# Performance work log

Hardware: AMD Instinct MI355X
Metric: run time of the kernel (lower is better)

The kernel has to match this reference:

```python
import jax, jax.numpy as jnp
import numpy as np
from jax import lax

B, S, D, T = 128, 512, 512, 64
OUT = 3


def setup_inputs() -> dict:
    key = jax.random.key(0)
    ks = jax.random.split(key, 16)
    sd = 0.05
    return {
        "e_all": jax.random.normal(ks[0], (B, S, D), jnp.float32),
        "e_last": jax.random.normal(ks[1], (1, B, D), jnp.float32),
        "target": jax.random.normal(ks[2], (B, T, OUT), jnp.float32),
        # attention params
        "Wa": jax.random.normal(ks[3], (D, D), jnp.float32) * sd,
        "ba": jnp.zeros((D,), jnp.float32),
        "Ua": jax.random.normal(ks[4], (D, D), jnp.float32) * sd,
        "bu": jnp.zeros((D,), jnp.float32),
        "Va_w": jax.random.normal(ks[5], (1, D), jnp.float32) * sd,
        "Va_b": jnp.zeros((1,), jnp.float32),
        # GRU params (PyTorch layout: [3D, in], gates order r,z,n)
        "W_ih": jax.random.normal(ks[6], (3 * D, D + OUT), jnp.float32) * sd,
        "b_ih": jnp.zeros((3 * D,), jnp.float32),
        "W_hh": jax.random.normal(ks[7], (3 * D, D), jnp.float32) * sd,
        "b_hh": jnp.zeros((3 * D,), jnp.float32),
        # output projection
        "W_out": jax.random.normal(ks[8], (OUT, D), jnp.float32) * sd,
        "b_out": jnp.zeros((OUT,), jnp.float32),
    }


def reference(e_all, e_last, target, Wa, ba, Ua, bu, Va_w, Va_b,
              W_ih, b_ih, W_hh, b_hh, W_out, b_out):
    # Precompute Ua(keys): keys are fixed across timesteps (same math as per-step).
    Uk = jnp.einsum('bsd,ed->bse', e_all, Ua) + bu        # [B,S,D]
    va = Va_w[0]                                          # [D]

    def step(h, x):
        # h: [B,D] decoder hidden; x: [B,3] decoder input (dropout is eval/identity)
        q = h @ Wa.T + ba                                  # [B,D]
        scores = jnp.einsum('bsd,d->bs', jnp.tanh(q[:, None, :] + Uk), va) + Va_b[0]
        w = jax.nn.softmax(scores, axis=-1)                # [B,S]
        ctx = jnp.einsum('bs,bsd->bd', w, e_all)           # [B,D]
        gin = jnp.concatenate([ctx, x], axis=-1)           # [B,D+3]  (attn first)
        gi = gin @ W_ih.T + b_ih                           # [B,3D]
        gh = h @ W_hh.T + b_hh                             # [B,3D]
        i_r, i_z, i_n = jnp.split(gi, 3, axis=-1)
        h_r, h_z, h_n = jnp.split(gh, 3, axis=-1)
        r = jax.nn.sigmoid(i_r + h_r)
        z = jax.nn.sigmoid(i_z + h_z)
        n = jnp.tanh(i_n + r * h_n)
        h_new = (1.0 - z) * n + z * h                      # [B,D]
        out = h_new @ W_out.T + b_out                      # [B,3]
        return h_new, (out, w)

    # teacher forcing: step 0 sees zeros, step i sees target[:, i-1]
    xs = jnp.concatenate([jnp.zeros((1, B, OUT), e_all.dtype),
                          jnp.swapaxes(target[:, :T - 1, :], 0, 1)], axis=0)  # [T,B,3]
    hT, (outs, attns) = lax.scan(step, e_last[0], xs)
    d_outputs = jnp.swapaxes(outs, 0, 1)     # [B,T,3]
    cross_attn = jnp.swapaxes(attns, 0, 1)   # [B,T,S]
    return d_outputs, hT[None], cross_attn
```

## Files before the change

kernel.cpp:

```cpp
#include <hip/hip_runtime.h>
#include <cstdint>

constexpr int BB = 128;
constexpr int SS = 512;
constexpr int DD = 512;
constexpr int TT = 64;
constexpr int OO = 3;

typedef __attribute__((ext_vector_type(8))) short bf16x8;
typedef __attribute__((ext_vector_type(4))) float f32x4;

__device__ __forceinline__ float tanh_fast(float x) {
  float e = __expf(2.0f * x);
  return 1.0f - 2.0f / (e + 1.0f);
}
__device__ __forceinline__ float sigmoid_fast(float x) {
  return 1.0f / (1.0f + __expf(-x));
}
__device__ __forceinline__ unsigned short f2bf(float f) {
  uint32_t u = __float_as_uint(f);
  uint32_t r = (u + 0x7FFFu + ((u >> 16) & 1u)) >> 16;
  return (unsigned short)r;
}
__device__ __forceinline__ float2 bfx2(uint32_t u) {
  float2 r;
  r.x = __uint_as_float(u << 16);
  r.y = __uint_as_float(u & 0xFFFF0000u);
  return r;
}

template<int BM, int BN, int BK, int TM, int TN>
__device__ __forceinline__ void gemm_body(
    const float* __restrict__ A, int lda,
    const float* __restrict__ Bw, int ldb,
    const float* __restrict__ bias,
    float* __restrict__ C, int ldc, int K) {
  constexpr int TX = BN / TN, TY = BM / TM;
  static_assert(TX * TY == 256, "tile/thread mismatch");
  __shared__ float As[BK][BM + 4];
  __shared__ float Bs[BK][BN + 4];
  const int tid = threadIdx.x;
  const int bm = blockIdx.y * BM, bn = blockIdx.x * BN;
  const int tx = tid % TX, ty = tid / TX;
  float acc[TM][TN];
#pragma unroll
  for (int i = 0; i < TM; ++i)
#pragma unroll
    for (int j = 0; j < TN; ++j) acc[i][j] = 0.f;

  for (int k0 = 0; k0 < K; k0 += BK) {
#pragma unroll
    for (int i = 0; i < BM * BK / 256; ++i) {
      int idx = tid + i * 256;
      int m = idx / BK, k = idx % BK;
      As[k][m] = A[(size_t)(bm + m) * lda + k0 + k];
    }
#pragma unroll
    for (int i = 0; i < BN * BK / 256; ++i) {
      int idx = tid + i * 256;
      int n = idx / BK, k = idx % BK;
      Bs[k][n] = Bw[(size_t)(bn + n) * ldb + k0 + k];
    }
    __syncthreads();
#pragma unroll
    for (int k = 0; k < BK; ++k) {
      float ra[TM], rb[TN];
#pragma unroll
      for (int i = 0; i < TM; ++i) ra[i] = As[k][ty * TM + i];
#pragma unroll
      for (int j = 0; j < TN; ++j) rb[j] = Bs[k][tx * TN + j];
#pragma unroll
      for (int i = 0; i < TM; ++i)
#pragma unroll
        for (int j = 0; j < TN; ++j) acc[i][j] += ra[i] * rb[j];
    }
    __syncthreads();
  }
#pragma unroll
  for (int i = 0; i < TM; ++i) {
    int m = bm + ty * TM + i;
#pragma unroll
    for (int j = 0; j < TN; ++j) {
      int n = bn + tx * TN + j;
      C[(size_t)m * ldc + n] = acc[i][j] + bias[n];
    }
  }
}

__global__ __launch_bounds__(256) void gemm_uk_mfma(
    const unsigned short* __restrict__ A, const unsigned short* __restrict__ Bw,
    const float* __restrict__ bias, unsigned short* __restrict__ Uk) {
  __shared__ unsigned short Asb[128 * 40];
  __shared__ unsigned short Bsb[128 * 40];
  const int tid = threadIdx.x;
  const int m0 = blockIdx.y * 128, n0 = blockIdx.x * 128;
  const int w = tid >> 6, l = tid & 63;
  const int wr = w >> 1, wc = w & 1;
  const int lm = l & 15, kg = l >> 4;

  f32x4 acc[4][4] = {};

  for (int kc = 0; kc < 512; kc += 32) {
    uint4 av[2], bv[2];
#pragma unroll
    for (int p = 0; p < 2; ++p) {
      int u = tid + p * 256;
      int r = u >> 2, ko = (u & 3) * 8;
      av[p] = *(const uint4*)(A + (size_t)(m0 + r) * 512 + kc + ko);
      bv[p] = *(const uint4*)(Bw + (size_t)(n0 + r) * 512 + kc + ko);
    }
    __syncthreads();
#pragma unroll
    for (int p = 0; p < 2; ++p) {
      int u = tid + p * 256;
      int r = u >> 2, ko = (u & 3) * 8;
      *(uint4*)&Asb[r * 40 + ko] = av[p];
      *(uint4*)&Bsb[r * 40 + ko] = bv[p];
    }
    __syncthreads();
    bf16x8 af[4], bfr[4];
#pragma unroll
    for (int i = 0; i < 4; ++i) {
      af[i]  = *(const bf16x8*)&Asb[(wr * 64 + i * 16 + lm) * 40 + kg * 8];
      bfr[i] = *(const bf16x8*)&Bsb[(wc * 64 + i * 16 + lm) * 40 + kg * 8];
    }
#pragma unroll
    for (int i = 0; i < 4; ++i)
#pragma unroll
      for (int j = 0; j < 4; ++j)
        acc[i][j] = __builtin_amdgcn_mfma_f32_16x16x32_bf16(af[i], bfr[j],
                                                            acc[i][j], 0, 0, 0);
  }

  const int row_base = m0 + wr * 64;
  const int col_base = n0 + wc * 64;
#pragma unroll
  for (int j = 0; j < 4; ++j) {
    const int col = col_base + j * 16 + lm;
    const float bu = bias[col];
#pragma unroll
    for (int i = 0; i < 4; ++i) {
      const int r0 = row_base + i * 16 + kg * 4;
#pragma unroll
      for (int rr = 0; rr < 4; ++rr)
        Uk[(size_t)(r0 + rr) * 512 + col] = f2bf(acc[i][j][rr] + bu);
    }
  }
}

__global__ __launch_bounds__(256) void conv_bf(const float* __restrict__ in,
                                               unsigned short* __restrict__ outp) {
  size_t idx = ((size_t)blockIdx.x * 256 + threadIdx.x) * 8;
  const float4* p = (const float4*)(in + idx);
  float4 a = p[0], b = p[1];
  uint4 r;
  r.x = f2bf(a.x) | ((uint32_t)f2bf(a.y) << 16);
  r.y = f2bf(a.z) | ((uint32_t)f2bf(a.w) << 16);
  r.z = f2bf(b.x) | ((uint32_t)f2bf(b.y) << 16);
  r.w = f2bf(b.z) | ((uint32_t)f2bf(b.w) << 16);
  *(uint4*)(outp + idx) = r;
}

__global__ void prep_wcat(const float* __restrict__ Wa,
                          const float* __restrict__ Whh,
                          uint32_t* __restrict__ Wcat) {
  int idx = blockIdx.x * 256 + threadIdx.x;
  int k = idx >> 10, j2 = idx & 1023;
  int j0 = 2 * j2;
  float v0 = (j0 < DD) ? Wa[(size_t)j0 * DD + k] : Whh[(size_t)(j0 - DD) * DD + k];
  float v1 = (j0 + 1 < DD) ? Wa[(size_t)(j0 + 1) * DD + k]
                           : Whh[(size_t)(j0 + 1 - DD) * DD + k];
  Wcat[idx] = (uint32_t)f2bf(v0) | ((uint32_t)f2bf(v1) << 16);
}

__global__ void prep_bcat(const float* __restrict__ ba,
                          const float* __restrict__ bhh,
                          float* __restrict__ bcat) {
  int j = blockIdx.x * 256 + threadIdx.x;
  bcat[j] = (j < DD) ? ba[j] : bhh[j - DD];
}

__device__ __forceinline__ void qgh_gemm(
    const float* __restrict__ hn_sh, const uint32_t* __restrict__ Wcat,
    const float* __restrict__ bcat, float* __restrict__ q,
    float* __restrict__ gh, int b, int tid) {
  float2 acc = {0.f, 0.f};
#pragma unroll 8
  for (int k = 0; k < DD; ++k) {
    float2 wv = bfx2(Wcat[(size_t)k * 1024 + tid]);
    float hv = hn_sh[k];
    acc.x += hv * wv.x;
    acc.y += hv * wv.y;
  }
  const int j0 = 2 * tid;
  acc.x += bcat[j0];
  acc.y += bcat[j0 + 1];
  if (j0 < DD) {
    q[(size_t)b * DD + j0] = acc.x;
    q[(size_t)b * DD + j0 + 1] = acc.y;
  } else {
    gh[(size_t)b * 3 * DD + j0 - DD] = acc.x;
    gh[(size_t)b * 3 * DD + j0 + 1 - DD] = acc.y;
  }
}

__global__ __launch_bounds__(1024) void qgh_init(
    const float* __restrict__ e_last, const uint32_t* __restrict__ Wcat,
    const float* __restrict__ bcat, float* __restrict__ h,
    float* __restrict__ q, float* __restrict__ gh) {
  const int b = blockIdx.x, tid = threadIdx.x;
  __shared__ float hn[DD];
  if (tid < DD) {
    float v = e_last[(size_t)b * DD + tid];
    hn[tid] = v;
    h[(size_t)b * DD + tid] = v;
  }
  __syncthreads();
  qgh_gemm(hn, Wcat, bcat, q, gh, b, tid);
}

__global__ __launch_bounds__(256) void attn_scores(
    const unsigned short* __restrict__ Uk_bf, const float* __restrict__ q,
    const float* __restrict__ va, const float* __restrict__ vb_p,
    float* __restrict__ scores) {
  const int b = blockIdx.y;
  const int s0 = blockIdx.x * 64;
  __shared__ float4 shq[DD / 4];
  __shared__ float4 shva[DD / 4];
  const int tid = threadIdx.x;
  if (tid < DD / 4) {
    shq[tid] = ((const float4*)(q + (size_t)b * DD))[tid];
    shva[tid] = ((const float4*)va)[tid];
  }
  __syncthreads();
  const float vb = vb_p[0];
  const int g = tid >> 4, l = tid & 15;
#pragma unroll
  for (int i = 0; i < 4; ++i) {
    const int s = s0 + 16 * i + g;
    const uint4* row = (const uint4*)(Uk_bf + ((size_t)b * SS + s) * DD);
    float acc = 0.f;
#pragma unroll
    for (int jj = 0; jj < 4; ++jj) {
      const int slot = l + 16 * jj;
      uint4 u = row[slot];
      float4 q0 = shq[slot * 2], q1 = shq[slot * 2 + 1];
      float4 v0 = shva[slot * 2], v1 = shva[slot * 2 + 1];
      float2 e0 = bfx2(u.x), e1 = bfx2(u.y), e2 = bfx2(u.z), e3 = bfx2(u.w);
      acc += v0.x * tanh_fast(q0.x + e0.x);
      acc += v0.y * tanh_fast(q0.y + e0.y);
      acc += v0.z * tanh_fast(q0.z + e1.x);
      acc += v0.w * tanh_fast(q0.w + e1.y);
      acc += v1.x * tanh_fast(q1.x + e2.x);
      acc += v1.y * tanh_fast(q1.y + e2.y);
      acc += v1.z * tanh_fast(q1.z + e3.x);
      acc += v1.w * tanh_fast(q1.w + e3.y);
    }
#pragma unroll
    for (int off = 8; off; off >>= 1) acc += __shfl_down(acc, off, 16);
    if (l == 0) scores[(size_t)b * SS + s] = acc + vb;
  }
}

__global__ __launch_bounds__(256) void attn_ctx(
    const unsigned short* __restrict__ e_bf, const float* __restrict__ scores,
    float* __restrict__ ctx, float* __restrict__ attn_out, int t) {
  const int b = blockIdx.y, dc = blockIdx.x;
  __shared__ float w[SS];
  __shared__ float red[8];
  __shared__ float part[16][132];
  const int tid = threadIdx.x;

  float v0 = scores[(size_t)b * SS + tid];
  float v1 = scores[(size_t)b * SS + 256 + tid];
  float m = fmaxf(v0, v1);
#pragma unroll
  for (int off = 32; off; off >>= 1) m = fmaxf(m, __shfl_xor(m, off));
  if ((tid & 63) == 0) red[tid >> 6] = m;
  __syncthreads();
  m = fmaxf(fmaxf(red[0], red[1]), fmaxf(red[2], red[3]));
  float e0 = __expf(v0 - m), e1 = __expf(v1 - m);
  float ss = e0 + e1;
#pragma unroll
  for (int off = 32; off; off >>= 1) ss += __shfl_xor(ss, off);
  __syncthreads();
  if ((tid & 63) == 0) red[tid >> 6] = ss;
  __syncthreads();
  const float inv = 1.f / (red[0] + red[1] + red[2] + red[3]);
  float w0 = e0 * inv, w1 = e1 * inv;
  w[tid] = w0;
  w[tid + 256] = w1;
  if (dc == 0) {
    float* ao = attn_out + ((size_t)b * TT + t) * SS;
    ao[tid] = w0;
    ao[tid + 256] = w1;
  }
  __syncthreads();

  {
    const int sl = tid & 15, sg = tid >> 4;
    const unsigned short* eb = e_bf + (size_t)b * SS * DD + dc * 128 + sl * 8;
    float a0 = 0.f, a1 = 0.f, a2 = 0.f, a3 = 0.f;
    float a4 = 0.f, a5 = 0.f, a6 = 0.f, a7 = 0.f;
    for (int s = sg * 32; s < sg * 32 + 32; ++s) {
      uint4 u = *(const uint4*)(eb + (size_t)s * DD);
      float ws = w[s];
      float2 p0 = bfx2(u.x), p1 = bfx2(u.y), p2 = bfx2(u.z), p3 = bfx2(u.w);
      a0 += ws * p0.x; a1 += ws * p0.y;
      a2 += ws * p1.x; a3 += ws * p1.y;
      a4 += ws * p2.x; a5 += ws * p2.y;
      a6 += ws * p3.x; a7 += ws * p3.y;
    }
    float* pr = &part[sg][sl * 8];
    pr[0] = a0; pr[1] = a1; pr[2] = a2; pr[3] = a3;
    pr[4] = a4; pr[5] = a5; pr[6] = a6; pr[7] = a7;
  }
  __syncthreads();
  if (tid < 128) {
    const int sl = tid >> 3, c = tid & 7;
    float r = 0.f;
#pragma unroll
    for (int sg = 0; sg < 16; ++sg) r += part[sg][sl * 8 + c];
    ctx[(size_t)b * DD + dc * 128 + sl * 8 + c] = r;
  }
}

__global__ __launch_bounds__(256) void gi_gemm(
    const float* __restrict__ ctx, const float* __restrict__ W_ih,
    const float* __restrict__ bih, float* __restrict__ gi) {
  gemm_body<16, 64, 32, 1, 4>(ctx, DD, W_ih, DD + OO, bih, gi, 3 * DD, DD);
}

__global__ __launch_bounds__(1024) void update_fused(
    const float* __restrict__ gi, float* __restrict__ gh,
    float* __restrict__ h,
    const float* __restrict__ W_ih, const float* __restrict__ target,
    const float* __restrict__ W_out, const float* __restrict__ b_out,
    const uint32_t* __restrict__ Wcat, const float* __restrict__ bcat,
    float* __restrict__ q,
    float* __restrict__ out_d, float* __restrict__ out_hT, int t) {
  const int b = blockIdx.x, tid = threadIdx.x;
  __shared__ float hn[DD];
  const int wid = tid >> 6, lane = tid & 63;

  if (tid < DD) {
    const int d = tid;
    float x0 = 0.f, x1 = 0.f, x2 = 0.f;
    if (t > 0) {
      const float* xp = target + ((size_t)b * TT + (t - 1)) * OO;
      x0 = xp[0]; x1 = xp[1]; x2 = xp[2];
    }
    const float* gib = gi + (size_t)b * 3 * DD;
    const float* ghb = gh + (size_t)b * 3 * DD;
    const float* w0 = W_ih + (size_t)d * (DD + OO) + DD;
    const float* w1 = W_ih + (size_t)(DD + d) * (DD + OO) + DD;
    const float* w2 = W_ih + (size_t)(2 * DD + d) * (DD + OO) + DD;
    float ir  = gib[d]          + x0 * w0[0] + x1 * w0[1] + x2 * w0[2];
    float iz  = gib[DD + d]     + x0 * w1[0] + x1 * w1[1] + x2 * w1[2];
    float in_ = gib[2 * DD + d] + x0 * w2[0] + x1 * w2[1] + x2 * w2[2];
    float r = sigmoid_fast(ir + ghb[d]);
    float z = sigmoid_fast(iz + ghb[DD + d]);
    float n = tanh_fast(in_ + r * ghb[2 * DD + d]);
    float hp = h[(size_t)b * DD + d];
    float hnew = (1.f - z) * n + z * hp;
    h[(size_t)b * DD + d] = hnew;
    hn[d] = hnew;
    if (t == TT - 1) out_hT[(size_t)b * DD + d] = hnew;
  }
  __syncthreads();

  if (wid < OO) {
    const float* wrow = W_out + (size_t)wid * DD;
    float acc = 0.f;
    for (int i = lane; i < DD; i += 64) acc += hn[i] * wrow[i];
#pragma unroll
    for (int off = 32; off; off >>= 1) acc += __shfl_xor(acc, off);
    if (lane == 0) out_d[((size_t)b * TT + t) * OO + wid] = acc + b_out[wid];
  }

  qgh_gemm(hn, Wcat, bcat, q, gh, b, tid);
}

extern "C" void kernel_launch(void* const* d_in, const int* in_sizes, int n_in,
                              void* d_out, int out_size, void* d_ws, size_t ws_size,
                              hipStream_t stream) {
  const float* e_all  = (const float*)d_in[0];
  const float* e_last = (const float*)d_in[1];
  const float* target = (const float*)d_in[2];
  const float* Wa     = (const float*)d_in[3];
  const float* ba     = (const float*)d_in[4];
  const float* Ua     = (const float*)d_in[5];
  const float* bu     = (const float*)d_in[6];
  const float* Va_w   = (const float*)d_in[7];
  const float* Va_b   = (const float*)d_in[8];
  const float* W_ih   = (const float*)d_in[9];
  const float* b_ih   = (const float*)d_in[10];
  const float* W_hh   = (const float*)d_in[11];
  const float* b_hh   = (const float*)d_in[12];
  const float* W_out  = (const float*)d_in[13];
  const float* b_out  = (const float*)d_in[14];

  float* out      = (float*)d_out;
  float* out_d    = out;
  float* out_hT   = out + (size_t)BB * TT * OO;
  float* out_attn = out_hT + (size_t)BB * DD;

  char* wsB = (char*)d_ws;
  unsigned short* Uk_bf = (unsigned short*)wsB;
  unsigned short* e_bf  = (unsigned short*)(wsB + (size_t)BB * SS * DD * 2);
  uint32_t* Wcat = (uint32_t*)(wsB + (size_t)BB * SS * DD * 4);
  unsigned short* Ua_bf = (unsigned short*)(wsB + (size_t)BB * SS * DD * 4 +
                                            (size_t)DD * 2048 * 2);
  float* fws = (float*)((char*)Ua_bf + (size_t)DD * DD * 2);
  float* bcat   = fws;
  float* scores = bcat + 2048;
  float* q    = scores + (size_t)BB * SS;
  float* h    = q + (size_t)BB * DD;
  float* ctx  = h + (size_t)BB * DD;
  float* gi   = ctx + (size_t)BB * DD;
  float* gh   = gi + (size_t)BB * 3 * DD;

  prep_wcat<<<(DD * 1024) / 256, 256, 0, stream>>>(Wa, W_hh, Wcat);
  prep_bcat<<<2048 / 256, 256, 0, stream>>>(ba, b_hh, bcat);
  conv_bf<<<(BB * SS * DD) / (8 * 256), 256, 0, stream>>>(e_all, e_bf);
  conv_bf<<<(DD * DD) / (8 * 256), 256, 0, stream>>>(Ua, Ua_bf);
  gemm_uk_mfma<<<dim3(DD / 128, (BB * SS) / 128), 256, 0, stream>>>(
      e_bf, Ua_bf, bu, Uk_bf);
  qgh_init<<<BB, 1024, 0, stream>>>(e_last, Wcat, bcat, h, q, gh);

  for (int t = 0; t < TT; ++t) {
    attn_scores<<<dim3(SS / 64, BB), 256, 0, stream>>>(Uk_bf, q, Va_w, Va_b,
                                                       scores);
    attn_ctx<<<dim3(4, BB), 256, 0, stream>>>(e_bf, scores, ctx, out_attn, t);
    gi_gemm<<<dim3(3 * DD / 64, BB / 16), 256, 0, stream>>>(ctx, W_ih, b_ih, gi);
    update_fused<<<BB, 1024, 0, stream>>>(gi, gh, h, W_ih, target, W_out, b_out,
                                          Wcat, bcat, q, out_d, out_hT, t);
  }
}
```

Before: 5.621 ms.

## Fuse per-step attention, q/gh projection and GRU into two kernels per timestep

Restructures the per-timestep pipeline from four launches to two. The first kernel computes q, scores, softmax and context for each batch row in one 1024-thread block, and a sibling block computes gh in parallel. The second kernel does the input-gate GEMV against a pre-transposed bf16 W_ih plus the GRU update, split across two blocks per row. The output projection is deferred one step, with a tail kernel for the final step. This removes launches and the global round trips for scores, q and gi, but has only 256 blocks per launch and moves W_ih to bf16, which adds rounding error.

```diff
diff --git a/kernel.cpp b/kernel.cpp
--- a/kernel.cpp
+++ b/kernel.cpp
@@ -27,64 +27,6 @@
   r.x = __uint_as_float(u << 16);
   r.y = __uint_as_float(u & 0xFFFF0000u);
   return r;
-}
-
-template<int BM, int BN, int BK, int TM, int TN>
-__device__ __forceinline__ void gemm_body(
-    const float* __restrict__ A, int lda,
-    const float* __restrict__ Bw, int ldb,
-    const float* __restrict__ bias,
-    float* __restrict__ C, int ldc, int K) {
-  constexpr int TX = BN / TN, TY = BM / TM;
-  static_assert(TX * TY == 256, "tile/thread mismatch");
-  __shared__ float As[BK][BM + 4];
-  __shared__ float Bs[BK][BN + 4];
-  const int tid = threadIdx.x;
-  const int bm = blockIdx.y * BM, bn = blockIdx.x * BN;
-  const int tx = tid % TX, ty = tid / TX;
-  float acc[TM][TN];
-#pragma unroll
-  for (int i = 0; i < TM; ++i)
-#pragma unroll
-    for (int j = 0; j < TN; ++j) acc[i][j] = 0.f;
-
-  for (int k0 = 0; k0 < K; k0 += BK) {
-#pragma unroll
-    for (int i = 0; i < BM * BK / 256; ++i) {
-      int idx = tid + i * 256;
-      int m = idx / BK, k = idx % BK;
-      As[k][m] = A[(size_t)(bm + m) * lda + k0 + k];
-    }
-#pragma unroll
-    for (int i = 0; i < BN * BK / 256; ++i) {
-      int idx = tid + i * 256;
-      int n = idx / BK, k = idx % BK;
-      Bs[k][n] = Bw[(size_t)(bn + n) * ldb + k0 + k];
-    }
-    __syncthreads();
-#pragma unroll
-    for (int k = 0; k < BK; ++k) {
-      float ra[TM], rb[TN];
-#pragma unroll
-      for (int i = 0; i < TM; ++i) ra[i] = As[k][ty * TM + i];
-#pragma unroll
-      for (int j = 0; j < TN; ++j) rb[j] = Bs[k][tx * TN + j];
-#pragma unroll
-      for (int i = 0; i < TM; ++i)
-#pragma unroll
-        for (int j = 0; j < TN; ++j) acc[i][j] += ra[i] * rb[j];
-    }
-    __syncthreads();
-  }
-#pragma unroll
-  for (int i = 0; i < TM; ++i) {
-    int m = bm + ty * TM + i;
-#pragma unroll
-    for (int j = 0; j < TN; ++j) {
-      int n = bn + tx * TN + j;
-      C[(size_t)m * ldc + n] = acc[i][j] + bias[n];
-    }
-  }
 }
 
 __global__ __launch_bounds__(256) void gemm_uk_mfma(
@@ -173,136 +115,164 @@
   Wcat[idx] = (uint32_t)f2bf(v0) | ((uint32_t)f2bf(v1) << 16);
 }
 
-__global__ void prep_bcat(const float* __restrict__ ba,
-                          const float* __restrict__ bhh,
-                          float* __restrict__ bcat) {
-  int j = blockIdx.x * 256 + threadIdx.x;
-  bcat[j] = (j < DD) ? ba[j] : bhh[j - DD];
-}
-
-__device__ __forceinline__ void qgh_gemm(
-    const float* __restrict__ hn_sh, const uint32_t* __restrict__ Wcat,
-    const float* __restrict__ bcat, float* __restrict__ q,
-    float* __restrict__ gh, int b, int tid) {
-  float2 acc = {0.f, 0.f};
+__global__ void prep_wihT(const float* __restrict__ W_ih,
+                          uint32_t* __restrict__ WihT) {
+  int idx = blockIdx.x * 256 + threadIdx.x;
+  int k = idx / 768, pp = idx % 768;
+  int p0 = 2 * pp;
+  float v0 = W_ih[(size_t)p0 * (DD + OO) + k];
+  float v1 = W_ih[(size_t)(p0 + 1) * (DD + OO) + k];
+  WihT[idx] = (uint32_t)f2bf(v0) | ((uint32_t)f2bf(v1) << 16);
+}
+
+__global__ __launch_bounds__(1024) void step_k1(
+    const unsigned short* __restrict__ Uk_bf,
+    const unsigned short* __restrict__ e_bf,
+    const uint32_t* __restrict__ Wcat,
+    const float* __restrict__ ba, const float* __restrict__ bhh,
+    const float* __restrict__ va, const float* __restrict__ vb_p,
+    const float* __restrict__ W_out, const float* __restrict__ b_out,
+    const float* __restrict__ h,
+    float* __restrict__ ctx, float* __restrict__ gh,
+    float* __restrict__ out_d, float* __restrict__ out_attn, int t) {
+  const int b = blockIdx.y;
+  const int tid = threadIdx.x;
+
+  __shared__ float hs[DD];
+  __shared__ __align__(16) float qsh[DD];
+  __shared__ __align__(16) float vash[DD];
+  __shared__ float w[SS];
+  __shared__ float red[16];
+  __shared__ float2 qp[4][256];
+  __shared__ float part[16][520];
+
+  if (tid < DD) hs[tid] = h[(size_t)b * DD + tid];
+  __syncthreads();
+
+  if (blockIdx.x == 1) {
+    if (tid < 768) {
+      const int j2 = 256 + tid;
+      float2 acc = {0.f, 0.f};
 #pragma unroll 8
-  for (int k = 0; k < DD; ++k) {
-    float2 wv = bfx2(Wcat[(size_t)k * 1024 + tid]);
-    float hv = hn_sh[k];
-    acc.x += hv * wv.x;
-    acc.y += hv * wv.y;
-  }
-  const int j0 = 2 * tid;
-  acc.x += bcat[j0];
-  acc.y += bcat[j0 + 1];
-  if (j0 < DD) {
-    q[(size_t)b * DD + j0] = acc.x;
-    q[(size_t)b * DD + j0 + 1] = acc.y;
-  } else {
-    gh[(size_t)b * 3 * DD + j0 - DD] = acc.x;
-    gh[(size_t)b * 3 * DD + j0 + 1 - DD] = acc.y;
-  }
-}
-
-__global__ __launch_bounds__(1024) void qgh_init(
-    const float* __restrict__ e_last, const uint32_t* __restrict__ Wcat,
-    const float* __restrict__ bcat, float* __restrict__ h,
-    float* __restrict__ q, float* __restrict__ gh) {
-  const int b = blockIdx.x, tid = threadIdx.x;
-  __shared__ float hn[DD];
-  if (tid < DD) {
-    float v = e_last[(size_t)b * DD + tid];
-    hn[tid] = v;
-    h[(size_t)b * DD + tid] = v;
-  }
-  __syncthreads();
-  qgh_gemm(hn, Wcat, bcat, q, gh, b, tid);
-}
-
-__global__ __launch_bounds__(256) void attn_scores(
-    const unsigned short* __restrict__ Uk_bf, const float* __restrict__ q,
-    const float* __restrict__ va, const float* __restrict__ vb_p,
-    float* __restrict__ scores) {
-  const int b = blockIdx.y;
-  const int s0 = blockIdx.x * 64;
-  __shared__ float4 shq[DD / 4];
-  __shared__ float4 shva[DD / 4];
-  const int tid = threadIdx.x;
-  if (tid < DD / 4) {
-    shq[tid] = ((const float4*)(q + (size_t)b * DD))[tid];
-    shva[tid] = ((const float4*)va)[tid];
-  }
-  __syncthreads();
-  const float vb = vb_p[0];
-  const int g = tid >> 4, l = tid & 15;
-#pragma unroll
-  for (int i = 0; i < 4; ++i) {
-    const int s = s0 + 16 * i + g;
-    const uint4* row = (const uint4*)(Uk_bf + ((size_t)b * SS + s) * DD);
+      for (int k = 0; k < DD; ++k) {
+        float2 wv = bfx2(Wcat[(size_t)k * 1024 + j2]);
+        float hv = hs[k];
+        acc.x += hv * wv.x;
+        acc.y += hv * wv.y;
+      }
+      const int j0 = 2 * tid;
+      gh[(size_t)b * 3 * DD + j0] = acc.x + bhh[j0];
+      gh[(size_t)b * 3 * DD + j0 + 1] = acc.y + bhh[j0 + 1];
+    }
+    return;
+  }
+
+  const int wid = tid >> 6, lane = tid & 63;
+
+  if (t > 0 && wid < OO) {
+    const float* wrow = W_out + (size_t)wid * DD;
     float acc = 0.f;
-#pragma unroll
-    for (int jj = 0; jj < 4; ++jj) {
-      const int slot = l + 16 * jj;
-      uint4 u = row[slot];
-      float4 q0 = shq[slot * 2], q1 = shq[slot * 2 + 1];
-      float4 v0 = shva[slot * 2], v1 = shva[slot * 2 + 1];
-      float2 e0 = bfx2(u.x), e1 = bfx2(u.y), e2 = bfx2(u.z), e3 = bfx2(u.w);
-      acc += v0.x * tanh_fast(q0.x + e0.x);
-      acc += v0.y * tanh_fast(q0.y + e0.y);
-      acc += v0.z * tanh_fast(q0.z + e1.x);
-      acc += v0.w * tanh_fast(q0.w + e1.y);
-      acc += v1.x * tanh_fast(q1.x + e2.x);
-      acc += v1.y * tanh_fast(q1.y + e2.y);
-      acc += v1.z * tanh_fast(q1.z + e3.x);
-      acc += v1.w * tanh_fast(q1.w + e3.y);
-    }
-#pragma unroll
-    for (int off = 8; off; off >>= 1) acc += __shfl_down(acc, off, 16);
-    if (l == 0) scores[(size_t)b * SS + s] = acc + vb;
-  }
-}
-
-__global__ __launch_bounds__(256) void attn_ctx(
-    const unsigned short* __restrict__ e_bf, const float* __restrict__ scores,
-    float* __restrict__ ctx, float* __restrict__ attn_out, int t) {
-  const int b = blockIdx.y, dc = blockIdx.x;
-  __shared__ float w[SS];
-  __shared__ float red[8];
-  __shared__ float part[16][132];
-  const int tid = threadIdx.x;
-
-  float v0 = scores[(size_t)b * SS + tid];
-  float v1 = scores[(size_t)b * SS + 256 + tid];
-  float m = fmaxf(v0, v1);
+    for (int i = lane; i < DD; i += 64) acc += hs[i] * wrow[i];
+#pragma unroll
+    for (int off = 32; off; off >>= 1) acc += __shfl_xor(acc, off);
+    if (lane == 0) out_d[((size_t)b * TT + (t - 1)) * OO + wid] = acc + b_out[wid];
+  }
+  if (tid < DD) vash[tid] = va[tid];
+
+  {
+    const int kh = tid >> 8, e2 = tid & 255;
+    float2 acc = {0.f, 0.f};
+    for (int k = kh * 128; k < kh * 128 + 128; ++k) {
+      float2 wv = bfx2(Wcat[(size_t)k * 1024 + e2]);
+      float hv = hs[k];
+      acc.x += hv * wv.x;
+      acc.y += hv * wv.y;
+    }
+    qp[kh][e2] = acc;
+  }
+  __syncthreads();
+  if (tid < 256) {
+    float2 r0 = qp[0][tid], r1 = qp[1][tid], r2 = qp[2][tid], r3 = qp[3][tid];
+    qsh[2 * tid] = r0.x + r1.x + r2.x + r3.x + ba[2 * tid];
+    qsh[2 * tid + 1] = r0.y + r1.y + r2.y + r3.y + ba[2 * tid + 1];
+  }
+  __syncthreads();
+
+  {
+    const float vb = vb_p[0];
+    const int g = tid >> 4, l = tid & 15;
+    const float4* q4 = (const float4*)qsh;
+    const float4* v4 = (const float4*)vash;
+#pragma unroll
+    for (int i = 0; i < 8; ++i) {
+      const int s = g + 64 * i;
+      const uint4* row = (const uint4*)(Uk_bf + ((size_t)b * SS + s) * DD);
+      float acc = 0.f;
+#pragma unroll
+      for (int jj = 0; jj < 4; ++jj) {
+        const int slot = l + 16 * jj;
+        uint4 u = row[slot];
+        float4 q0 = q4[slot * 2], q1 = q4[slot * 2 + 1];
+        float4 v0 = v4[slot * 2], v1 = v4[slot * 2 + 1];
+        float2 e0 = bfx2(u.x), e1 = bfx2(u.y), e2 = bfx2(u.z), e3 = bfx2(u.w);
+        acc += v0.x * tanh_fast(q0.x + e0.x);
+        acc += v0.y * tanh_fast(q0.y + e0.y);
+        acc += v0.z * tanh_fast(q0.z + e1.x);
+        acc += v0.w * tanh_fast(q0.w + e1.y);
+        acc += v1.x * tanh_fast(q1.x + e2.x);
+        acc += v1.y * tanh_fast(q1.y + e2.y);
+        acc += v1.z * tanh_fast(q1.z + e3.x);
+        acc += v1.w * tanh_fast(q1.w + e3.y);
+      }
+#pragma unroll
+      for (int off = 8; off; off >>= 1) acc += __shfl_down(acc, off, 16);
+      if (l == 0) w[s] = acc + vb;
+    }
+  }
+  __syncthreads();
+
+  float v = (tid < SS) ? w[tid] : -3.4e38f;
+  float m = v;
 #pragma unroll
   for (int off = 32; off; off >>= 1) m = fmaxf(m, __shfl_xor(m, off));
-  if ((tid & 63) == 0) red[tid >> 6] = m;
-  __syncthreads();
-  m = fmaxf(fmaxf(red[0], red[1]), fmaxf(red[2], red[3]));
-  float e0 = __expf(v0 - m), e1 = __expf(v1 - m);
-  float ss = e0 + e1;
-#pragma unroll
-  for (int off = 32; off; off >>= 1) ss += __shfl_xor(ss, off);
-  __syncthreads();
-  if ((tid & 63) == 0) red[tid >> 6] = ss;
-  __syncthreads();
-  const float inv = 1.f / (red[0] + red[1] + red[2] + red[3]);
-  float w0 = e0 * inv, w1 = e1 * inv;
-  w[tid] = w0;
-  w[tid + 256] = w1;
-  if (dc == 0) {
-    float* ao = attn_out + ((size_t)b * TT + t) * SS;
-    ao[tid] = w0;
-    ao[tid + 256] = w1;
+  if (lane == 0) red[wid] = m;
+  __syncthreads();
+  if (tid < 16) {
+    float mm = red[tid];
+#pragma unroll
+    for (int off = 8; off; off >>= 1) mm = fmaxf(mm, __shfl_xor(mm, off, 16));
+    red[tid] = mm;
+  }
+  __syncthreads();
+  m = red[0];
+  float e_ = (tid < SS) ? __expf(v - m) : 0.f;
+  float ssum = e_;
+#pragma unroll
+  for (int off = 32; off; off >>= 1) ssum += __shfl_xor(ssum, off);
+  __syncthreads();
+  if (lane == 0) red[wid] = ssum;
+  __syncthreads();
+  if (tid < 16) {
+    float s2 = red[tid];
+#pragma unroll
+    for (int off = 8; off; off >>= 1) s2 += __shfl_xor(s2, off, 16);
+    red[tid] = s2;
+  }
+  __syncthreads();
+  const float inv = 1.f / red[0];
+  if (tid < SS) {
+    float wv = e_ * inv;
+    w[tid] = wv;
+    out_attn[((size_t)b * TT + t) * SS + tid] = wv;
   }
   __syncthreads();
 
   {
-    const int sl = tid & 15, sg = tid >> 4;
-    const unsigned short* eb = e_bf + (size_t)b * SS * DD + dc * 128 + sl * 8;
+    const int ss = tid >> 6, slot = tid & 63;
+    const unsigned short* eb = e_bf + (size_t)b * SS * DD + slot * 8;
     float a0 = 0.f, a1 = 0.f, a2 = 0.f, a3 = 0.f;
     float a4 = 0.f, a5 = 0.f, a6 = 0.f, a7 = 0.f;
-    for (int s = sg * 32; s < sg * 32 + 32; ++s) {
+    for (int s = ss * 32; s < ss * 32 + 32; ++s) {
       uint4 u = *(const uint4*)(eb + (size_t)s * DD);
       float ws = w[s];
       float2 p0 = bfx2(u.x), p1 = bfx2(u.y), p2 = bfx2(u.z), p3 = bfx2(u.w);
@@ -311,74 +281,87 @@
       a4 += ws * p2.x; a5 += ws * p2.y;
       a6 += ws * p3.x; a7 += ws * p3.y;
     }
-    float* pr = &part[sg][sl * 8];
+    float* pr = &part[ss][slot * 8];
     pr[0] = a0; pr[1] = a1; pr[2] = a2; pr[3] = a3;
     pr[4] = a4; pr[5] = a5; pr[6] = a6; pr[7] = a7;
   }
   __syncthreads();
-  if (tid < 128) {
-    const int sl = tid >> 3, c = tid & 7;
+  if (tid < DD) {
     float r = 0.f;
 #pragma unroll
-    for (int sg = 0; sg < 16; ++sg) r += part[sg][sl * 8 + c];
-    ctx[(size_t)b * DD + dc * 128 + sl * 8 + c] = r;
-  }
-}
-
-__global__ __launch_bounds__(256) void gi_gemm(
-    const float* __restrict__ ctx, const float* __restrict__ W_ih,
-    const float* __restrict__ bih, float* __restrict__ gi) {
-  gemm_body<16, 64, 32, 1, 4>(ctx, DD, W_ih, DD + OO, bih, gi, 3 * DD, DD);
-}
-
-__global__ __launch_bounds__(1024) void update_fused(
-    const float* __restrict__ gi, float* __restrict__ gh,
-    float* __restrict__ h,
-    const float* __restrict__ W_ih, const float* __restrict__ target,
-    const float* __restrict__ W_out, const float* __restrict__ b_out,
-    const uint32_t* __restrict__ Wcat, const float* __restrict__ bcat,
-    float* __restrict__ q,
-    float* __restrict__ out_d, float* __restrict__ out_hT, int t) {
-  const int b = blockIdx.x, tid = threadIdx.x;
-  __shared__ float hn[DD];
-  const int wid = tid >> 6, lane = tid & 63;
-
-  if (tid < DD) {
-    const int d = tid;
-    float x0 = 0.f, x1 = 0.f, x2 = 0.f;
-    if (t > 0) {
-      const float* xp = target + ((size_t)b * TT + (t - 1)) * OO;
-      x0 = xp[0]; x1 = xp[1]; x2 = xp[2];
-    }
-    const float* gib = gi + (size_t)b * 3 * DD;
+    for (int ss = 0; ss < 16; ++ss) r += part[ss][tid];
+    ctx[(size_t)b * DD + tid] = r;
+  }
+}
+
+__global__ __launch_bounds__(1024) void step_k2(
+    const float* __restrict__ ctx, const uint32_t* __restrict__ WihT,
+    const float* __restrict__ W_ih, const float* __restrict__ bih,
+    const float* __restrict__ target, const float* __restrict__ gh,
+    float* __restrict__ h, int t) {
+  const int half = blockIdx.x, b = blockIdx.y;
+  const int tid = threadIdx.x;
+  __shared__ float cs[DD];
+  __shared__ float gis[768];
+  __shared__ float xs[3];
+
+  if (tid < DD) cs[tid] = ctx[(size_t)b * DD + tid];
+  if (tid < 3) xs[tid] = (t > 0) ? target[((size_t)b * TT + (t - 1)) * OO + tid] : 0.f;
+  __syncthreads();
+
+  if (tid < 384) {
+    const int gate = tid >> 7, pi = tid & 127;
+    const int ppair = gate * 256 + half * 128 + pi;
+    const int p0 = 2 * ppair;
+    float2 acc = {0.f, 0.f};
+#pragma unroll 8
+    for (int k = 0; k < DD; ++k) {
+      float2 wv = bfx2(WihT[(size_t)k * 768 + ppair]);
+      float cv = cs[k];
+      acc.x += cv * wv.x;
+      acc.y += cv * wv.y;
+    }
+    const float* wx0 = W_ih + (size_t)p0 * (DD + OO) + DD;
+    const float* wx1 = W_ih + (size_t)(p0 + 1) * (DD + OO) + DD;
+    acc.x += xs[0] * wx0[0] + xs[1] * wx0[1] + xs[2] * wx0[2];
+    acc.y += xs[0] * wx1[0] + xs[1] * wx1[1] + xs[2] * wx1[2];
+    const int l0 = gate * 256 + 2 * pi;
+    gis[l0] = acc.x + bih[p0];
+    gis[l0 + 1] = acc.y + bih[p0 + 1];
+  }
+  __syncthreads();
+
+  if (tid < 256) {
+    const int d = half * 256 + tid;
     const float* ghb = gh + (size_t)b * 3 * DD;
-    const float* w0 = W_ih + (size_t)d * (DD + OO) + DD;
-    const float* w1 = W_ih + (size_t)(DD + d) * (DD + OO) + DD;
-    const float* w2 = W_ih + (size_t)(2 * DD + d) * (DD + OO) + DD;
-    float ir  = gib[d]          + x0 * w0[0] + x1 * w0[1] + x2 * w0[2];
-    float iz  = gib[DD + d]     + x0 * w1[0] + x1 * w1[1] + x2 * w1[2];
-    float in_ = gib[2 * DD + d] + x0 * w2[0] + x1 * w2[1] + x2 * w2[2];
+    float ir = gis[tid], iz = gis[256 + tid], in_ = gis[512 + tid];
     float r = sigmoid_fast(ir + ghb[d]);
     float z = sigmoid_fast(iz + ghb[DD + d]);
     float n = tanh_fast(in_ + r * ghb[2 * DD + d]);
     float hp = h[(size_t)b * DD + d];
-    float hnew = (1.f - z) * n + z * hp;
-    h[(size_t)b * DD + d] = hnew;
-    hn[d] = hnew;
-    if (t == TT - 1) out_hT[(size_t)b * DD + d] = hnew;
-  }
-  __syncthreads();
-
+    h[(size_t)b * DD + d] = (1.f - z) * n + z * hp;
+  }
+}
+
+__global__ __launch_bounds__(512) void out_tail(
+    const float* __restrict__ h, const float* __restrict__ W_out,
+    const float* __restrict__ b_out, float* __restrict__ out_d,
+    float* __restrict__ out_hT) {
+  const int b = blockIdx.x, tid = threadIdx.x;
+  __shared__ float hs[DD];
+  float hv = h[(size_t)b * DD + tid];
+  hs[tid] = hv;
+  out_hT[(size_t)b * DD + tid] = hv;
+  __syncthreads();
+  const int wid = tid >> 6, lane = tid & 63;
   if (wid < OO) {
     const float* wrow = W_out + (size_t)wid * DD;
     float acc = 0.f;
-    for (int i = lane; i < DD; i += 64) acc += hn[i] * wrow[i];
+    for (int i = lane; i < DD; i += 64) acc += hs[i] * wrow[i];
 #pragma unroll
     for (int off = 32; off; off >>= 1) acc += __shfl_xor(acc, off);
-    if (lane == 0) out_d[((size_t)b * TT + t) * OO + wid] = acc + b_out[wid];
-  }
-
-  qgh_gemm(hn, Wcat, bcat, q, gh, b, tid);
+    if (lane == 0) out_d[((size_t)b * TT + (TT - 1)) * OO + wid] = acc + b_out[wid];
+  }
 }
 
 extern "C" void kernel_launch(void* const* d_in, const int* in_sizes, int n_in,
@@ -409,31 +392,29 @@
   unsigned short* Uk_bf = (unsigned short*)wsB;
   unsigned short* e_bf  = (unsigned short*)(wsB + (size_t)BB * SS * DD * 2);
   uint32_t* Wcat = (uint32_t*)(wsB + (size_t)BB * SS * DD * 4);
-  unsigned short* Ua_bf = (unsigned short*)(wsB + (size_t)BB * SS * DD * 4 +
-                                            (size_t)DD * 2048 * 2);
-  float* fws = (float*)((char*)Ua_bf + (size_t)DD * DD * 2);
-  float* bcat   = fws;
-  float* scores = bcat + 2048;
-  float* q    = scores + (size_t)BB * SS;
-  float* h    = q + (size_t)BB * DD;
-  float* ctx  = h + (size_t)BB * DD;
-  float* gi   = ctx + (size_t)BB * DD;
-  float* gh   = gi + (size_t)BB * 3 * DD;
-
-  prep_wcat<<<(DD * 1024) / 256, 256, 0, stream>>>(Wa, W_hh, Wcat);
-  prep_bcat<<<2048 / 256, 256, 0, stream>>>(ba, b_hh, bcat);
+  char* overlap = wsB + (size_t)BB * SS * DD * 4 + (size_t)DD * 1024 * 4;
+  unsigned short* Ua_bf = (unsigned short*)overlap;
+  uint32_t* WihT = (uint32_t*)overlap;
+  float* fws = (float*)(overlap + (size_t)DD * 768 * 4);
+  float* h   = fws;
+  float* ctx = h + (size_t)BB * DD;
+  float* gh  = ctx + (size_t)BB * DD;
+
   conv_bf<<<(BB * SS * DD) / (8 * 256), 256, 0, stream>>>(e_all, e_bf);
   conv_bf<<<(DD * DD) / (8 * 256), 256, 0, stream>>>(Ua, Ua_bf);
+  prep_wcat<<<(DD * 1024) / 256, 256, 0, stream>>>(Wa, W_hh, Wcat);
   gemm_uk_mfma<<<dim3(DD / 128, (BB * SS) / 128), 256, 0, stream>>>(
       e_bf, Ua_bf, bu, Uk_bf);
-  qgh_init<<<BB, 1024, 0, stream>>>(e_last, Wcat, bcat, h, q, gh);
+  prep_wihT<<<(DD * 768) / 256, 256, 0, stream>>>(W_ih, WihT);
+  hipMemcpyAsync(h, e_last, (size_t)BB * DD * sizeof(float),
+                 hipMemcpyDeviceToDevice, stream);
 
   for (int t = 0; t < TT; ++t) {
-    attn_scores<<<dim3(SS / 64, BB), 256, 0, stream>>>(Uk_bf, q, Va_w, Va_b,
-                                                       scores);
-    attn_ctx<<<dim3(4, BB), 256, 0, stream>>>(e_bf, scores, ctx, out_attn, t);
-    gi_gemm<<<dim3(3 * DD / 64, BB / 16), 256, 0, stream>>>(ctx, W_ih, b_ih, gi);
-    update_fused<<<BB, 1024, 0, stream>>>(gi, gh, h, W_ih, target, W_out, b_out,
-                                          Wcat, bcat, q, out_d, out_hT, t);
-  }
-}
+    step_k1<<<dim3(2, BB), 1024, 0, stream>>>(
+        Uk_bf, e_bf, Wcat, ba, b_hh, Va_w, Va_b, W_out, b_out,
+        h, ctx, gh, out_d, out_attn, t);
+    step_k2<<<dim3(2, BB), 1024, 0, stream>>>(
+        ctx, WihT, W_ih, b_ih, target, gh, h, t);
+  }
+  out_tail<<<BB, 512, 0, stream>>>(h, W_out, b_out, out_d, out_hT);
+}
```

Result: slower. 7.041 ms (+25.3%).
